# Performance work log

Hardware: AMD Instinct MI355X
Metric: run time of the kernel (lower is better)

## Reference

```python
import jax, jax.numpy as jnp
import numpy as np

LAMBDA_COLOR = 10.0


def _neighbors(x, p):
    """Patch-unfold: x [B,C,H,W] -> [B, P*P, C, H, W] of zero-padded shifted copies.
    Matches conv3d with diagonal one-hot [P^2,1,1,P,P] weights, padding (0,pad,pad)."""
    pad = (p - 1) // 2
    B, C, H, W = x.shape
    xp = jnp.pad(x, ((0, 0), (0, 0), (pad, pad), (pad, pad)))
    shifts = [xp[:, :, i:i + H, j:j + W] for i in range(p) for j in range(p)]
    return jnp.stack(shifts, axis=1)


def _spatial_grid(img_size):
    # np.mgrid[-1:1+eps:2/(S-1), -1:1+eps:2/(S-1)] -> [2, S, S] (y-coords, x-coords)
    lin = jnp.linspace(-1.0, 1.0, img_size, dtype=jnp.float32)
    gy, gx = jnp.meshgrid(lin, lin, indexing='ij')
    return jnp.stack([gy, gx], axis=0)[None]  # [1, 2, S, S]


def setup_inputs() -> dict:
    key = jax.random.key(0)
    k1, k2 = jax.random.split(key)
    B, S, P = 16, 256, 7
    flow = jax.random.normal(k1, (B, 2, S, S), dtype=jnp.float32)
    image = jax.random.uniform(k2, (B, 3, S, S), dtype=jnp.float32)
    return {"flow": flow, "image": image, "img_size": S, "patch_size": P}


def reference(flow, image, img_size, patch_size):
    flow = flow * img_size                                  # [B,2,H,W]
    grid = _spatial_grid(img_size)                          # [1,2,H,W]

    flow_nb = _neighbors(flow, patch_size)                  # [B,P2,2,H,W]
    img_nb = _neighbors(image, patch_size)                  # [B,P2,3,H,W]
    grid_nb = _neighbors(grid, patch_size)                  # [1,P2,2,H,W]

    im_w = jnp.sum((image[:, None] - img_nb) ** 2, axis=2)  # [B,P2,H,W]
    sp_w = jnp.sum((grid[:, None] - grid_nb) ** 2, axis=2)  # [1,P2,H,W]
    fl = jnp.sum((flow_nb - flow[:, None]) ** 2, axis=2)    # [B,P2,H,W]

    return jnp.mean(fl * jnp.exp(-(im_w * LAMBDA_COLOR + sp_w)))
```

## Files before the change

### kernel.cpp

```cpp
#include <hip/hip_runtime.h>


#define S_DIM 256
#define PAD 3
#define TILE_X 64
#define TILE_Y 16
#define CX 4
#define QX (TILE_X / CX)
#define HALO_X (TILE_X + 2*PAD)
#define HALO_Y (TILE_Y + PAD)
#define LSTRIDE 72
#define N_TERMS 51380224.0f

__global__ void init_out_kernel(float* out) { out[0] = 0.0f; }

__global__ __launch_bounds__(256) void flow_reg_loss_kernel(
    const float* __restrict__ flow,
    const float* __restrict__ image,
    float* __restrict__ out)
{
    __shared__ float sm[5][HALO_Y][LSTRIDE];
    __shared__ float wave_sums[4];

    const int b   = blockIdx.z;
    const int tx0 = blockIdx.x * TILE_X;
    const int ty0 = blockIdx.y * TILE_Y;
    const int tid = threadIdx.y * QX + threadIdx.x;

    const float* img_b = image + (size_t)b * 3 * S_DIM * S_DIM;
    const float* flw_b = flow  + (size_t)b * 2 * S_DIM * S_DIM;

    for (int e = tid; e < HALO_Y * HALO_X; e += 256) {
        const int ly = e / HALO_X;
        const int lx = e - ly * HALO_X;
        const int gy = ty0 + ly;
        const int gx = tx0 - PAD + lx;
        float i0 = 0.f, i1 = 0.f, i2 = 0.f, f0 = 0.f, f1 = 0.f;
        if ((unsigned)gy < S_DIM && (unsigned)gx < S_DIM) {
            const int g = gy * S_DIM + gx;
            i0 = img_b[0 * S_DIM * S_DIM + g];
            i1 = img_b[1 * S_DIM * S_DIM + g];
            i2 = img_b[2 * S_DIM * S_DIM + g];
            f0 = flw_b[0 * S_DIM * S_DIM + g] * 256.0f;
            f1 = flw_b[1 * S_DIM * S_DIM + g] * 256.0f;
        }
        sm[0][ly][lx] = i0;
        sm[1][ly][lx] = i1;
        sm[2][ly][lx] = i2;
        sm[3][ly][lx] = f0;
        sm[4][ly][lx] = f1;
    }
    __syncthreads();

    const int qx = threadIdx.x;
    const int ty = threadIdx.y;
    const int xb = qx * CX;
    const int y  = ty0 + ty;
    const int x0 = tx0 + xb;

    const float step = 2.0f / 255.0f;
    const float K2 = step * step;

    float acc = 0.0f;
    float ic0[CX], ic1[CX], ic2[CX], fc0[CX], fc1[CX];

    {
        float r[5][12];
#pragma unroll
        for (int c = 0; c < 5; ++c) {
            const float4 a  = *(const float4*)&sm[c][ty][xb];
            const float4 b4 = *(const float4*)&sm[c][ty][xb + 4];
            const float4 c4 = *(const float4*)&sm[c][ty][xb + 8];
            r[c][0] = a.x;  r[c][1] = a.y;  r[c][2]  = a.z;  r[c][3]  = a.w;
            r[c][4] = b4.x; r[c][5] = b4.y; r[c][6]  = b4.z; r[c][7]  = b4.w;
            r[c][8] = c4.x; r[c][9] = c4.y; r[c][10] = c4.z; r[c][11] = c4.w;
        }
#pragma unroll
        for (int i = 0; i < CX; ++i) {
            ic0[i] = r[0][3 + i]; ic1[i] = r[1][3 + i]; ic2[i] = r[2][3 + i];
            fc0[i] = r[3][3 + i]; fc1[i] = r[4][3 + i];
        }
#pragma unroll
        for (int dx = 1; dx <= PAD; ++dx) {
            const float spw_in = K2 * (float)(dx * dx);
#pragma unroll
            for (int i = 0; i < CX; ++i) {
                const int j = i + dx + 3;
                const float d0 = ic0[i] - r[0][j];
                const float d1 = ic1[i] - r[1][j];
                const float d2 = ic2[i] - r[2][j];
                const float imw = d0 * d0 + d1 * d1 + d2 * d2;
                const float e0 = r[3][j] - fc0[i];
                const float e1 = r[4][j] - fc1[i];
                const float fl2 = e0 * e0 + e1 * e1;
                const float w = ((unsigned)(x0 + i + dx) < S_DIM) ? 1.0f : 0.0f;
                acc += (w * fl2) * __expf(-(imw * 10.0f + spw_in));
            }
        }
    }

#pragma unroll
    for (int dy = 1; dy <= PAD; ++dy) {
        const int ny = ty + dy;
        const bool yin = (y + dy) < S_DIM;
        float r[5][12];
#pragma unroll
        for (int c = 0; c < 5; ++c) {
            const float4 a  = *(const float4*)&sm[c][ny][xb];
            const float4 b4 = *(const float4*)&sm[c][ny][xb + 4];
            const float4 c4 = *(const float4*)&sm[c][ny][xb + 8];
            r[c][0] = a.x;  r[c][1] = a.y;  r[c][2]  = a.z;  r[c][3]  = a.w;
            r[c][4] = b4.x; r[c][5] = b4.y; r[c][6]  = b4.z; r[c][7]  = b4.w;
            r[c][8] = c4.x; r[c][9] = c4.y; r[c][10] = c4.z; r[c][11] = c4.w;
        }
#pragma unroll
        for (int dx = -PAD; dx <= PAD; ++dx) {
            const float spw_in = K2 * (float)(dy * dy + dx * dx);
#pragma unroll
            for (int i = 0; i < CX; ++i) {
                const int j = i + dx + 3;
                const float d0 = ic0[i] - r[0][j];
                const float d1 = ic1[i] - r[1][j];
                const float d2 = ic2[i] - r[2][j];
                const float imw = d0 * d0 + d1 * d1 + d2 * d2;
                const float e0 = r[3][j] - fc0[i];
                const float e1 = r[4][j] - fc1[i];
                const float fl2 = e0 * e0 + e1 * e1;
                const float w = (yin && (unsigned)(x0 + i + dx) < S_DIM) ? 1.0f : 0.0f;
                acc += (w * fl2) * __expf(-(imw * 10.0f + spw_in));
            }
        }
    }

    const int ny_in = 7 - max(0, 3 - y) - max(0, y - (S_DIM - 1 - 3));
    const float gyc = -1.0f + step * (float)y;
    float oob = 0.0f;
#pragma unroll
    for (int i = 0; i < CX; ++i) {
        const int xg = x0 + i;
        const int nx_in = 7 - max(0, 3 - xg) - max(0, xg - (S_DIM - 1 - 3));
        const float n_oob = (float)(49 - ny_in * nx_in);
        const float gxc = -1.0f + step * (float)xg;
        const float g2c = gyc * gyc + gxc * gxc;
        const float imw_c = ic0[i] * ic0[i] + ic1[i] * ic1[i] + ic2[i] * ic2[i];
        const float fl_c  = fc0[i] * fc0[i] + fc1[i] * fc1[i];
        oob += (n_oob * fl_c) * __expf(-(imw_c * 10.0f + g2c));
    }

    float acc_all = 2.0f * acc + oob;
#pragma unroll
    for (int off = 32; off > 0; off >>= 1)
        acc_all += __shfl_down(acc_all, off, 64);
    if ((tid & 63) == 0) wave_sums[tid >> 6] = acc_all;
    __syncthreads();
    if (tid == 0) {
        const float s = wave_sums[0] + wave_sums[1] + wave_sums[2] + wave_sums[3];
        atomicAdd(out, s * (1.0f / N_TERMS));
    }
}

extern "C" void kernel_launch(void* const* d_in, const int* in_sizes, int n_in,
                              void* d_out, int out_size, void* d_ws, size_t ws_size,
                              hipStream_t stream) {
    const float* flow  = (const float*)d_in[0];
    const float* image = (const float*)d_in[1];
    float* out = (float*)d_out;

    init_out_kernel<<<1, 1, 0, stream>>>(out);

    dim3 grid(S_DIM / TILE_X, S_DIM / TILE_Y, 16);
    dim3 block(QX, TILE_Y);
    flow_reg_loss_kernel<<<grid, block, 0, stream>>>(flow, image, out);
}
```

Measured before the change: 91.15 us.

## Replace LDS halo tiling with direct buffer loads and a two-stage reduction

Drops the shared-memory halo staging and its barrier. Each wave now handles one full image row and loads its neighbour rows straight from global memory with raw buffer loads, relying on the hardware range check to return zeros past the buffer end and on the existing masks elsewhere. The exponent is rewritten as a single exp2 with log2e folded into an fma. The flow scale of 256 is moved into the final normalisation constant. The atomic accumulation and its init kernel are replaced by per-block partial sums plus a small reduce kernel. The cost is redundant global or cache reads of neighbour rows in place of the LDS reuse.

New measurement: 84.93 us. 1.07x faster.

```diff
diff --git a/kernel.cpp b/kernel.cpp
--- a/kernel.cpp
+++ b/kernel.cpp
@@ -2,89 +2,92 @@
 
 
 #define S_DIM 256
-#define PAD 3
-#define TILE_X 64
-#define TILE_Y 16
-#define CX 4
-#define QX (TILE_X / CX)
-#define HALO_X (TILE_X + 2*PAD)
-#define HALO_Y (TILE_Y + PAD)
-#define LSTRIDE 72
+#define LOG2E 1.4426950408889634f
+#define C10L2E (-14.426950408889634f)
 #define N_TERMS 51380224.0f
+#define FINAL_SCALE (65536.0f / N_TERMS)
 
-__global__ void init_out_kernel(float* out) { out[0] = 0.0f; }
+typedef float v4f __attribute__((ext_vector_type(4)));
+typedef int   v4i __attribute__((ext_vector_type(4)));
 
-__global__ __launch_bounds__(256) void flow_reg_loss_kernel(
+__device__ v4f llvm_amdgcn_raw_buffer_load_v4f32(v4i rsrc, int voffset,
+                                                 int soffset, int aux)
+    __asm("llvm.amdgcn.raw.buffer.load.v4f32");
+
+__device__ inline v4i make_srd(const void* p, unsigned bytes) {
+    union { v4i v; unsigned u[4]; } s;
+    s.u[0] = (unsigned)(unsigned long long)p;
+    s.u[1] = (unsigned)(((unsigned long long)p) >> 32);
+    s.u[2] = bytes;
+    s.u[3] = 0x00020000u;
+    return s.v;
+}
+
+__global__ __launch_bounds__(256, 4) void flow_reg_loss_kernel(
     const float* __restrict__ flow,
     const float* __restrict__ image,
-    float* __restrict__ out)
+    float* __restrict__ partial)
 {
-    __shared__ float sm[5][HALO_Y][LSTRIDE];
     __shared__ float wave_sums[4];
 
-    const int b   = blockIdx.z;
-    const int tx0 = blockIdx.x * TILE_X;
-    const int ty0 = blockIdx.y * TILE_Y;
-    const int tid = threadIdx.y * QX + threadIdx.x;
+    const int lane = threadIdx.x;
+    const int wy   = threadIdx.y;
+    const int y    = blockIdx.x * 4 + wy;
+    const int b    = blockIdx.z;
+    const int x0   = lane * 4;
 
-    const float* img_b = image + (size_t)b * 3 * S_DIM * S_DIM;
-    const float* flw_b = flow  + (size_t)b * 2 * S_DIM * S_DIM;
+    const v4i srdI = make_srd(image, 16u * 3u * 65536u * 4u);
+    const v4i srdF = make_srd(flow,  16u * 2u * 65536u * 4u);
 
-    for (int e = tid; e < HALO_Y * HALO_X; e += 256) {
-        const int ly = e / HALO_X;
-        const int lx = e - ly * HALO_X;
-        const int gy = ty0 + ly;
-        const int gx = tx0 - PAD + lx;
-        float i0 = 0.f, i1 = 0.f, i2 = 0.f, f0 = 0.f, f1 = 0.f;
-        if ((unsigned)gy < S_DIM && (unsigned)gx < S_DIM) {
-            const int g = gy * S_DIM + gx;
-            i0 = img_b[0 * S_DIM * S_DIM + g];
-            i1 = img_b[1 * S_DIM * S_DIM + g];
-            i2 = img_b[2 * S_DIM * S_DIM + g];
-            f0 = flw_b[0 * S_DIM * S_DIM + g] * 256.0f;
-            f1 = flw_b[1 * S_DIM * S_DIM + g] * 256.0f;
-        }
-        sm[0][ly][lx] = i0;
-        sm[1][ly][lx] = i1;
-        sm[2][ly][lx] = i2;
-        sm[3][ly][lx] = f0;
-        sm[4][ly][lx] = f1;
-    }
-    __syncthreads();
-
-    const int qx = threadIdx.x;
-    const int ty = threadIdx.y;
-    const int xb = qx * CX;
-    const int y  = ty0 + ty;
-    const int x0 = tx0 + xb;
+    const int rowx = x0 * 4 - 12;
+    const int ib = b * 786432;
+    const int fb = b * 524288;
 
     const float step = 2.0f / 255.0f;
-    const float K2 = step * step;
+    const float K2L2E = step * step * LOG2E;
 
     float acc = 0.0f;
-    float ic0[CX], ic1[CX], ic2[CX], fc0[CX], fc1[CX];
+    float ic0[4], ic1[4], ic2[4], fc0[4], fc1[4];
+
+#define LOAD_ROW(r, yy)                                                        \
+    do {                                                                       \
+        const int ro = (yy) * 1024 + rowx;                                     \
+        _Pragma("unroll")                                                      \
+        for (int c = 0; c < 3; ++c) {                                          \
+            const int v = ib + c * 262144 + ro;                                \
+            const v4f a  = llvm_amdgcn_raw_buffer_load_v4f32(srdI, v, 0, 0);   \
+            const v4f b4 = llvm_amdgcn_raw_buffer_load_v4f32(srdI, v, 16, 0);  \
+            const v4f c4 = llvm_amdgcn_raw_buffer_load_v4f32(srdI, v, 32, 0);  \
+            r[c][0] = a.x;  r[c][1] = a.y;  r[c][2]  = a.z;  r[c][3]  = a.w;   \
+            r[c][4] = b4.x; r[c][5] = b4.y; r[c][6]  = b4.z; r[c][7]  = b4.w;  \
+            r[c][8] = c4.x; r[c][9] = c4.y; r[c][10] = c4.z; r[c][11] = c4.w;  \
+        }                                                                      \
+        _Pragma("unroll")                                                      \
+        for (int c = 0; c < 2; ++c) {                                          \
+            const int v = fb + c * 262144 + ro;                                \
+            const v4f a  = llvm_amdgcn_raw_buffer_load_v4f32(srdF, v, 0, 0);   \
+            const v4f b4 = llvm_amdgcn_raw_buffer_load_v4f32(srdF, v, 16, 0);  \
+            const v4f c4 = llvm_amdgcn_raw_buffer_load_v4f32(srdF, v, 32, 0);  \
+            r[3+c][0] = a.x;  r[3+c][1] = a.y;  r[3+c][2]  = a.z;              \
+            r[3+c][3] = a.w;  r[3+c][4] = b4.x; r[3+c][5]  = b4.y;             \
+            r[3+c][6] = b4.z; r[3+c][7] = b4.w; r[3+c][8]  = c4.x;             \
+            r[3+c][9] = c4.y; r[3+c][10] = c4.z; r[3+c][11] = c4.w;            \
+        }                                                                      \
+    } while (0)
 
     {
         float r[5][12];
+        LOAD_ROW(r, y);
 #pragma unroll
-        for (int c = 0; c < 5; ++c) {
-            const float4 a  = *(const float4*)&sm[c][ty][xb];
-            const float4 b4 = *(const float4*)&sm[c][ty][xb + 4];
-            const float4 c4 = *(const float4*)&sm[c][ty][xb + 8];
-            r[c][0] = a.x;  r[c][1] = a.y;  r[c][2]  = a.z;  r[c][3]  = a.w;
-            r[c][4] = b4.x; r[c][5] = b4.y; r[c][6]  = b4.z; r[c][7]  = b4.w;
-            r[c][8] = c4.x; r[c][9] = c4.y; r[c][10] = c4.z; r[c][11] = c4.w;
-        }
-#pragma unroll
-        for (int i = 0; i < CX; ++i) {
+        for (int i = 0; i < 4; ++i) {
             ic0[i] = r[0][3 + i]; ic1[i] = r[1][3 + i]; ic2[i] = r[2][3 + i];
             fc0[i] = r[3][3 + i]; fc1[i] = r[4][3 + i];
         }
 #pragma unroll
-        for (int dx = 1; dx <= PAD; ++dx) {
-            const float spw_in = K2 * (float)(dx * dx);
+        for (int dx = 1; dx <= 3; ++dx) {
+            const float c2 = -K2L2E * (float)(dx * dx);
 #pragma unroll
-            for (int i = 0; i < CX; ++i) {
+            for (int i = 0; i < 4; ++i) {
                 const int j = i + dx + 3;
                 const float d0 = ic0[i] - r[0][j];
                 const float d1 = ic1[i] - r[1][j];
@@ -94,30 +97,21 @@
                 const float e1 = r[4][j] - fc1[i];
                 const float fl2 = e0 * e0 + e1 * e1;
                 const float w = ((unsigned)(x0 + i + dx) < S_DIM) ? 1.0f : 0.0f;
-                acc += (w * fl2) * __expf(-(imw * 10.0f + spw_in));
+                acc += (w * fl2) * __builtin_amdgcn_exp2f(fmaf(imw, C10L2E, c2));
             }
         }
     }
 
 #pragma unroll
-    for (int dy = 1; dy <= PAD; ++dy) {
-        const int ny = ty + dy;
+    for (int dy = 1; dy <= 3; ++dy) {
+        float r[5][12];
+        LOAD_ROW(r, y + dy);
         const bool yin = (y + dy) < S_DIM;
-        float r[5][12];
 #pragma unroll
-        for (int c = 0; c < 5; ++c) {
-            const float4 a  = *(const float4*)&sm[c][ny][xb];
-            const float4 b4 = *(const float4*)&sm[c][ny][xb + 4];
-            const float4 c4 = *(const float4*)&sm[c][ny][xb + 8];
-            r[c][0] = a.x;  r[c][1] = a.y;  r[c][2]  = a.z;  r[c][3]  = a.w;
-            r[c][4] = b4.x; r[c][5] = b4.y; r[c][6]  = b4.z; r[c][7]  = b4.w;
-            r[c][8] = c4.x; r[c][9] = c4.y; r[c][10] = c4.z; r[c][11] = c4.w;
-        }
+        for (int dx = -3; dx <= 3; ++dx) {
+            const float c2 = -K2L2E * (float)(dy * dy + dx * dx);
 #pragma unroll
-        for (int dx = -PAD; dx <= PAD; ++dx) {
-            const float spw_in = K2 * (float)(dy * dy + dx * dx);
-#pragma unroll
-            for (int i = 0; i < CX; ++i) {
+            for (int i = 0; i < 4; ++i) {
                 const int j = i + dx + 3;
                 const float d0 = ic0[i] - r[0][j];
                 const float d1 = ic1[i] - r[1][j];
@@ -127,7 +121,7 @@
                 const float e1 = r[4][j] - fc1[i];
                 const float fl2 = e0 * e0 + e1 * e1;
                 const float w = (yin && (unsigned)(x0 + i + dx) < S_DIM) ? 1.0f : 0.0f;
-                acc += (w * fl2) * __expf(-(imw * 10.0f + spw_in));
+                acc += (w * fl2) * __builtin_amdgcn_exp2f(fmaf(imw, C10L2E, c2));
             }
         }
     }
@@ -136,7 +130,7 @@
     const float gyc = -1.0f + step * (float)y;
     float oob = 0.0f;
 #pragma unroll
-    for (int i = 0; i < CX; ++i) {
+    for (int i = 0; i < 4; ++i) {
         const int xg = x0 + i;
         const int nx_in = 7 - max(0, 3 - xg) - max(0, xg - (S_DIM - 1 - 3));
         const float n_oob = (float)(49 - ny_in * nx_in);
@@ -144,18 +138,38 @@
         const float g2c = gyc * gyc + gxc * gxc;
         const float imw_c = ic0[i] * ic0[i] + ic1[i] * ic1[i] + ic2[i] * ic2[i];
         const float fl_c  = fc0[i] * fc0[i] + fc1[i] * fc1[i];
-        oob += (n_oob * fl_c) * __expf(-(imw_c * 10.0f + g2c));
+        oob += (n_oob * fl_c) *
+               __builtin_amdgcn_exp2f(fmaf(imw_c, C10L2E, -g2c * LOG2E));
     }
 
     float acc_all = 2.0f * acc + oob;
 #pragma unroll
     for (int off = 32; off > 0; off >>= 1)
         acc_all += __shfl_down(acc_all, off, 64);
-    if ((tid & 63) == 0) wave_sums[tid >> 6] = acc_all;
+    if (lane == 0) wave_sums[wy] = acc_all;
     __syncthreads();
-    if (tid == 0) {
-        const float s = wave_sums[0] + wave_sums[1] + wave_sums[2] + wave_sums[3];
-        atomicAdd(out, s * (1.0f / N_TERMS));
+    if (lane == 0 && wy == 0) {
+        partial[blockIdx.z * gridDim.x + blockIdx.x] =
+            (wave_sums[0] + wave_sums[1]) + (wave_sums[2] + wave_sums[3]);
+    }
+}
+
+__global__ __launch_bounds__(256) void reduce_kernel(
+    const float* __restrict__ partial, float* __restrict__ out)
+{
+    __shared__ float wave_sums[4];
+    const int t = threadIdx.x;
+    const v4f* p4 = (const v4f*)partial;
+    const v4f v = p4[t];
+    float s = (v.x + v.y) + (v.z + v.w);
+#pragma unroll
+    for (int off = 32; off > 0; off >>= 1)
+        s += __shfl_down(s, off, 64);
+    if ((t & 63) == 0) wave_sums[t >> 6] = s;
+    __syncthreads();
+    if (t == 0) {
+        out[0] = ((wave_sums[0] + wave_sums[1]) + (wave_sums[2] + wave_sums[3]))
+                 * FINAL_SCALE;
     }
 }
 
@@ -165,10 +179,10 @@
     const float* flow  = (const float*)d_in[0];
     const float* image = (const float*)d_in[1];
     float* out = (float*)d_out;
+    float* partial = (float*)d_ws;
 
-    init_out_kernel<<<1, 1, 0, stream>>>(out);
-
-    dim3 grid(S_DIM / TILE_X, S_DIM / TILE_Y, 16);
-    dim3 block(QX, TILE_Y);
-    flow_reg_loss_kernel<<<grid, block, 0, stream>>>(flow, image, out);
+    dim3 grid(64, 1, 16);
+    dim3 block(64, 4);
+    flow_reg_loss_kernel<<<grid, block, 0, stream>>>(flow, image, partial);
+    reduce_kernel<<<1, 256, 0, stream>>>(partial, out);
 }
```
